# Optimization experiments

Measured on AMD Instinct MI355X. Metric: run time of the kernel, lower is better.

The kernel has to match this reference:

```python
import jax, jax.numpy as jnp
import numpy as np

B, T, DIM = 8, 1024, 2048
H, NKV, HD = 16, 4, 128
G = H // NKV          # query heads per kv head
BASE = 10000.0
EPS = 1e-6
SCALE = HD ** -0.5


def _rope_tables(seqlen):
    inv = 1.0 / (BASE ** (np.arange(0, HD, 2, dtype=np.float32) / HD))  # [HD/2]
    t = np.arange(seqlen, dtype=np.float32)
    f = np.outer(t, inv)  # [T, HD/2]
    return jnp.asarray(np.cos(f)), jnp.asarray(np.sin(f))


def _rms_norm(x):
    return x * jax.lax.rsqrt(jnp.mean(x * x, axis=-1, keepdims=True) + EPS)


def _rope(x, cos, sin):
    # x: [B, heads, T, HD]; cos/sin broadcast over batch and heads
    x1, x2 = x[..., : HD // 2], x[..., HD // 2 :]
    return jnp.concatenate([x1 * cos - x2 * sin, x2 * cos + x1 * sin], axis=-1)


def setup_inputs() -> dict:
    key = jax.random.key(0)
    ks = jax.random.split(key, 6)
    s = 1.0 / np.sqrt(DIM)
    return {
        "x": jax.random.normal(ks[0], (B, T, DIM), dtype=jnp.float32),
        "Wq": jax.random.normal(ks[1], (DIM, DIM), dtype=jnp.float32) * s,
        "Wk": jax.random.normal(ks[2], (NKV * HD, DIM), dtype=jnp.float32) * s,
        "Wv": jax.random.normal(ks[3], (NKV * HD, DIM), dtype=jnp.float32) * s,
        "Wproj": jax.random.normal(ks[4], (DIM, DIM), dtype=jnp.float32) * s,
        "q_gain": jnp.ones((H,), dtype=jnp.float32),
    }


def reference(x, Wq, Wk, Wv, Wproj, q_gain):
    bsz, seqlen, dim = x.shape
    # projections -> [B, heads, T, HD]
    q = (x @ Wq.T).reshape(bsz, seqlen, H, HD).transpose(0, 2, 1, 3)
    k = (x @ Wk.T).reshape(bsz, seqlen, NKV, HD).transpose(0, 2, 1, 3)
    v = (x @ Wv.T).reshape(bsz, seqlen, NKV, HD).transpose(0, 2, 1, 3)

    cos, sin = _rope_tables(seqlen)
    cos, sin = cos[None, None], sin[None, None]
    q = _rope(_rms_norm(q), cos, sin) * q_gain[None, :, None, None]
    k = _rope(_rms_norm(k), cos, sin)

    # GQA: group query heads instead of materializing repeated k/v
    qg = q.reshape(bsz, NKV, G, seqlen, HD)
    scores = jnp.einsum("bngtd,bnsd->bngts", qg, k) * SCALE  # [B,NKV,G,T,T]
    causal = jnp.tril(jnp.ones((seqlen, seqlen), dtype=bool))
    scores = jnp.where(causal, scores, jnp.finfo(scores.dtype).min)
    p = jax.nn.softmax(scores, axis=-1)
    y = jnp.einsum("bngts,bnsd->bngtd", p, v)  # [B,NKV,G,T,HD]
    y = y.transpose(0, 3, 1, 2, 4).reshape(bsz, seqlen, dim)

    # XSA: subtract self-value projection per kv head
    y_g = y.reshape(bsz, seqlen, NKV, G, HD)
    v_t = v.transpose(0, 2, 1, 3)  # [B,T,NKV,HD]
    vn = v_t / (jnp.linalg.norm(v_t, axis=-1, keepdims=True) + 1e-8)
    vn = vn[:, :, :, None, :]  # broadcast over group dim
    proj_comp = jnp.sum(y_g * vn, axis=-1, keepdims=True) * vn
    y = (y_g - proj_comp).reshape(bsz, seqlen, dim)

    return y @ Wproj.T
```

## Files before the change

### kernel.cpp

```cpp
#include <hip/hip_runtime.h>
#include <stdint.h>

#define T_SEQ 1024

typedef _Float16 f16x8 __attribute__((ext_vector_type(8)));
typedef _Float16 f16x2 __attribute__((ext_vector_type(2)));
typedef float f32x4 __attribute__((ext_vector_type(4)));

typedef __attribute__((address_space(1))) const uint8_t* gptr_t;
typedef __attribute__((address_space(3))) uint8_t* lptr_t;

__device__ __forceinline__ void gload16(const _Float16* g, _Float16* l) {
  __builtin_amdgcn_global_load_lds((gptr_t)g, (lptr_t)l, 16, 0, 0);
}

__global__ __launch_bounds__(256) void convert_all(
    const float* __restrict__ x, const float* __restrict__ Wq,
    const float* __restrict__ Wk, const float* __restrict__ Wv,
    const float* __restrict__ Wp, _Float16* __restrict__ xh,
    _Float16* __restrict__ wqh, _Float16* __restrict__ wkh,
    _Float16* __restrict__ wvh, _Float16* __restrict__ wph) {
  int i = blockIdx.x * 256 + threadIdx.x;
  const float* in;
  _Float16* out;
  int base;
  if (i < 2097152)      { in = x;  out = xh;  base = 0; }
  else if (i < 2621440) { in = Wq; out = wqh; base = 2097152; }
  else if (i < 2752512) { in = Wk; out = wkh; base = 2621440; }
  else if (i < 2883584) { in = Wv; out = wvh; base = 2752512; }
  else                  { in = Wp; out = wph; base = 2883584; }
  int j = i - base;
  const float4* p = (const float4*)in + (size_t)j * 2;
  float4 a = p[0], b = p[1];
  f16x8 o;
  o[0] = (_Float16)a.x; o[1] = (_Float16)a.y; o[2] = (_Float16)a.z; o[3] = (_Float16)a.w;
  o[4] = (_Float16)b.x; o[5] = (_Float16)b.y; o[6] = (_Float16)b.z; o[7] = (_Float16)b.w;
  ((f16x8*)out)[j] = o;
}

template <typename OutT>
__global__ __launch_bounds__(512, 2) void gemm256(
    const _Float16* __restrict__ A, const _Float16* __restrict__ B,
    OutT* __restrict__ C0, int ldc0, int nb0,
    OutT* __restrict__ C1, int ldc1, int nbn) {
  __shared__ _Float16 As[2][256][64];
  __shared__ _Float16 Bs[2][256][64];
  const int tid = threadIdx.x;
  const int wave = tid >> 6, lane = tid & 63;
  const int lm = lane & 15, lq = lane >> 4;
  const int wm = wave >> 2, wn = wave & 3;

  const int qx = (int)gridDim.x >> 3;
  const int swz = ((int)blockIdx.x & 7) * qx + ((int)blockIdx.x >> 3);
  const int bm = swz / nbn, bn = swz % nbn;

  const int r8 = lane >> 3;
  const int csw = ((lane & 7) ^ r8) * 8;
  const _Float16* Asrc = A + (size_t)(bm * 256 + wave * 16 + r8) * 2048 + csw;
  const _Float16* Bsrc = B + (size_t)(bn * 256 + wave * 16 + r8) * 2048 + csw;

  f32x4 acc[8][4];
#pragma unroll
  for (int m = 0; m < 8; m++)
#pragma unroll
    for (int n = 0; n < 4; n++) acc[m][n] = (f32x4){0.f, 0.f, 0.f, 0.f};

  f16x8 af[4][2], bf[4][2];

  auto stageA = [&](int t, int h) {
    const _Float16* s = Asrc + (size_t)h * 128 * 2048 + t * 64;
    _Float16* d = &As[t & 1][h * 128 + wave * 16][0];
    gload16(s, d);
    gload16(s + (size_t)8 * 2048, d + 8 * 64);
  };
  auto stageB = [&](int t, int h) {
    const _Float16* s = Bsrc + (size_t)h * 128 * 2048 + t * 64;
    _Float16* d = &Bs[t & 1][h * 128 + wave * 16][0];
    gload16(s, d);
    gload16(s + (size_t)8 * 2048, d + 8 * 64);
  };
  auto lda = [&](int b, int mh) {
#pragma unroll
    for (int m = 0; m < 4; m++)
#pragma unroll
      for (int ks = 0; ks < 2; ks++)
        af[m][ks] = *(const f16x8*)&As[b][wm * 128 + mh * 64 + m * 16 + lm]
                                      [(((ks * 4 + lq)) ^ (lm & 7)) * 8];
  };
  auto ldb = [&](int b, int nh) {
#pragma unroll
    for (int n = 0; n < 2; n++)
#pragma unroll
      for (int ks = 0; ks < 2; ks++)
        bf[nh * 2 + n][ks] = *(const f16x8*)&Bs[b][wn * 64 + nh * 32 + n * 16 + lm]
                                               [(((ks * 4 + lq)) ^ (lm & 7)) * 8];
  };
  auto mfmaQ = [&](int mh, int nh) {
    __builtin_amdgcn_s_setprio(1);
#pragma unroll
    for (int m = 0; m < 4; m++)
#pragma unroll
      for (int n = 0; n < 2; n++)
#pragma unroll
        for (int ks = 0; ks < 2; ks++)
          acc[mh * 4 + m][nh * 2 + n] = __builtin_amdgcn_mfma_f32_16x16x32_f16(
              af[m][ks], bf[nh * 2 + n][ks], acc[mh * 4 + m][nh * 2 + n], 0, 0, 0);
    __builtin_amdgcn_s_setprio(0);
  };

#define BAR() __builtin_amdgcn_s_barrier()
#define BARX()                                         \
  do {                                                 \
    asm volatile("s_waitcnt lgkmcnt(0)" ::: "memory"); \
    __builtin_amdgcn_s_barrier();                      \
  } while (0)

  stageA(0, 0); stageA(0, 1);
  stageB(0, 0); stageB(0, 1);
  stageB(1, 0); stageB(1, 1);
  asm volatile("s_waitcnt vmcnt(4)" ::: "memory");
  BAR();

  const int NT = 32;
  for (int j = 0; j < NT / 2; ++j) {
    const int t1 = 2 * j + 1, t2 = 2 * j + 2, t3 = 2 * j + 3;
    const bool s2 = t2 < NT, s3 = t3 < NT;
    lda(0, 0); ldb(0, 0); stageA(t1, 0);
    mfmaQ(0, 0);
    ldb(0, 1); stageA(t1, 1);
    mfmaQ(0, 1);
    lda(0, 1);
    mfmaQ(1, 0);
    BARX();
    if (s2) { stageB(t2, 0); stageB(t2, 1); }
    mfmaQ(1, 1);
    if (s2) { asm volatile("s_waitcnt vmcnt(4)" ::: "memory"); }
    else    { asm volatile("s_waitcnt vmcnt(0)" ::: "memory"); }
    BAR();
    lda(1, 0); ldb(1, 0); if (s2) stageA(t2, 0);
    mfmaQ(0, 0);
    ldb(1, 1); if (s2) stageA(t2, 1);
    mfmaQ(0, 1);
    lda(1, 1);
    mfmaQ(1, 0);
    BARX();
    if (s3) { stageB(t3, 0); stageB(t3, 1); }
    mfmaQ(1, 1);
    asm volatile("s_waitcnt vmcnt(4)" ::: "memory");
    BAR();
  }
#undef BAR
#undef BARX

  OutT* C;
  int ldc, cb;
  if (bn < nb0) { C = C0; ldc = ldc0; cb = bn * 256; }
  else          { C = C1; ldc = ldc1; cb = (bn - nb0) * 256; }
#pragma unroll
  for (int m = 0; m < 8; m++) {
    size_t gr = (size_t)(bm * 256 + wm * 128 + m * 16 + lq * 4);
#pragma unroll
    for (int n = 0; n < 4; n++) {
      int gc = cb + wn * 64 + n * 16 + lm;
#pragma unroll
      for (int r = 0; r < 4; r++)
        C[(gr + r) * ldc + gc] = (OutT)acc[m][n][r];
    }
  }
}

__global__ __launch_bounds__(256) void transpose16(const _Float16* __restrict__ in,
                                                   _Float16* __restrict__ out) {
  __shared__ _Float16 Ts[64][72];
  int tr = blockIdx.x * 64, tc = blockIdx.y * 64;
  int r0 = threadIdx.x >> 3, c8 = (threadIdx.x & 7) * 8;
#pragma unroll
  for (int i = 0; i < 2; i++) {
    int r = r0 + i * 32;
    *(f16x8*)&Ts[r][c8] = *(const f16x8*)&in[(size_t)(tr + r) * 1024 + tc + c8];
  }
  __syncthreads();
#pragma unroll
  for (int i = 0; i < 2; i++) {
    int oc = r0 + i * 32;
    f16x8 o;
#pragma unroll
    for (int j = 0; j < 8; j++) o[j] = Ts[c8 + j][oc];
    *(f16x8*)&out[(size_t)(tc + oc) * 8192 + tr + c8] = o;
  }
}

__global__ __launch_bounds__(256) void rmsrope_all(_Float16* __restrict__ qh,
                                                   _Float16* __restrict__ kvb,
                                                   const float* __restrict__ gain) {
  int gw = blockIdx.x * 4 + (threadIdx.x >> 6);
  int lane = threadIdx.x & 63;
  _Float16* row;
  int t;
  float g = 1.0f;
  if (gw < 131072) {
    int h = gw & 15;
    t = (gw >> 4) & 1023;
    row = qh + (size_t)gw * 128;
    g = gain[h] * 0.08838834764831845f * 1.4426950408889634f;
  } else {
    int gk = gw - 131072;
    t = (gk >> 2) & 1023;
    row = kvb + (size_t)(gk >> 2) * 1024 + (gk & 3) * 128;
  }
  float x1 = (float)row[lane], x2 = (float)row[lane + 64];
  float ss = x1 * x1 + x2 * x2;
#pragma unroll
  for (int m = 1; m < 64; m <<= 1) ss += __shfl_xor(ss, m);
  float scale = rsqrtf(ss * (1.0f / 128.0f) + 1e-6f) * g;
  float inv = exp2f((float)lane * -0.2076205059304601f);
  float ang = (float)t * inv;
  float c = cosf(ang), s = sinf(ang);
  row[lane]      = (_Float16)((x1 * c - x2 * s) * scale);
  row[lane + 64] = (_Float16)((x2 * c + x1 * s) * scale);
}

__global__ __launch_bounds__(256, 2) void attn_mfma(const _Float16* __restrict__ q,
                                                    const _Float16* __restrict__ k,
                                                    const _Float16* __restrict__ vT,
                                                    _Float16* __restrict__ y) {
  __shared__ _Float16 Ks[2][4][64][32];
  __shared__ _Float16 VTs[2][2][128][32];
  __shared__ _Float16 Ps[4][32][64];
  int h = blockIdx.y, b = blockIdx.z;
  int kvh = h >> 2;
  int tid = threadIdx.x, wave = tid >> 6, lane = tid & 63;
  int lm = lane & 15, lq = lane >> 4;
  int srow = lane >> 2, scol = (lane & 3) * 8;

  for (int pass = 0; pass < 2; ++pass) {
    int qt = pass ? (int)blockIdx.x : 7 - (int)blockIdx.x;

    f16x8 qf[2][4];
#pragma unroll
    for (int mt = 0; mt < 2; mt++) {
      const _Float16* qp =
          q + ((size_t)((b * T_SEQ + qt * 128 + wave * 32 + mt * 16 + lm) * 16 + h)) * 128 +
          lq * 8;
#pragma unroll
      for (int ks = 0; ks < 4; ks++) qf[mt][ks] = *(const f16x8*)(qp + ks * 32);
    }

    f32x4 O[2][8];
#pragma unroll
    for (int mt = 0; mt < 2; mt++)
#pragma unroll
      for (int i = 0; i < 8; i++) O[mt][i] = (f32x4){0.f, 0.f, 0.f, 0.f};
    float mrow[2][4], lrow[2][4];
#pragma unroll
    for (int mt = 0; mt < 2; mt++)
#pragma unroll
      for (int r = 0; r < 4; r++) { mrow[mt][r] = -1e30f; lrow[mt][r] = 0.f; }

    const _Float16* kg =
        k + (size_t)(b * T_SEQ + srow) * 1024 + kvh * 128 + wave * 32 + scol;
    const _Float16* vg =
        vT + (size_t)(kvh * 128 + (wave >> 1) * 64 + srow) * 8192 + b * T_SEQ +
        (wave & 1) * 32 + scol;

    int wrow = qt * 128 + wave * 32;
    int nit = (qt + 1) * 2;

#pragma unroll
    for (int i = 0; i < 4; i++) {
      gload16(kg + (size_t)i * 16 * 1024, &Ks[0][wave][i * 16][0]);
      gload16(vg + (size_t)i * 16 * 8192, &VTs[0][wave & 1][(wave >> 1) * 64 + i * 16][0]);
    }
    kg += (size_t)64 * 1024;
    vg += 64;
    asm volatile("s_waitcnt vmcnt(0)" ::: "memory");
    __builtin_amdgcn_s_barrier();

    for (int it = 0; it < nit; ++it) {
      int cur = it & 1;
      int s0 = it * 64;
      if (it + 1 < nit) {
#pragma unroll
        for (int i = 0; i < 4; i++) {
          gload16(kg + (size_t)i * 16 * 1024, &Ks[cur ^ 1][wave][i * 16][0]);
          gload16(vg + (size_t)i * 16 * 8192,
                  &VTs[cur ^ 1][wave & 1][(wave >> 1) * 64 + i * 16][0]);
        }
        kg += (size_t)64 * 1024;
        vg += 64;
      }

      f32x4 S[2][4];
#pragma unroll
      for (int mt = 0; mt < 2; mt++)
#pragma unroll
        for (int ct = 0; ct < 4; ct++) S[mt][ct] = (f32x4){0.f, 0.f, 0.f, 0.f};
      __builtin_amdgcn_s_setprio(1);
#pragma unroll
      for (int ct = 0; ct < 4; ct++)
#pragma unroll
        for (int ks = 0; ks < 4; ks++) {
          f16x8 bfr = *(const f16x8*)&Ks[cur][ks][ct * 16 + lm][lq * 8];
          S[0][ct] = __builtin_amdgcn_mfma_f32_16x16x32_f16(qf[0][ks], bfr, S[0][ct], 0, 0, 0);
          S[1][ct] = __builtin_amdgcn_mfma_f32_16x16x32_f16(qf[1][ks], bfr, S[1][ct], 0, 0, 0);
        }
      __builtin_amdgcn_s_setprio(0);

      float p[2][4][4], al[2][4];
#pragma unroll
      for (int mt = 0; mt < 2; mt++) {
        bool need_mask = (s0 + 63 > wrow + mt * 16);
#pragma unroll
        for (int r = 0; r < 4; r++) {
          int grow = wrow + mt * 16 + lq * 4 + r;
          float mx = -1e30f;
#pragma unroll
          for (int ct = 0; ct < 4; ct++) {
            float sv = S[mt][ct][r];
            if (need_mask && (s0 + ct * 16 + lm > grow)) sv = -1e30f;
            p[mt][r][ct] = sv;
            mx = fmaxf(mx, sv);
          }
#pragma unroll
          for (int m = 1; m < 16; m <<= 1) mx = fmaxf(mx, __shfl_xor(mx, m));
          float mn = fmaxf(mrow[mt][r], mx);
          float a = exp2f(mrow[mt][r] - mn);
          mrow[mt][r] = mn;
          float rs = 0.f;
#pragma unroll
          for (int ct = 0; ct < 4; ct++) {
            float pv = exp2f(p[mt][r][ct] - mn);
            p[mt][r][ct] = pv;
            rs += pv;
          }
#pragma unroll
          for (int m = 1; m < 16; m <<= 1) rs += __shfl_xor(rs, m);
          lrow[mt][r] = lrow[mt][r] * a + rs;
          al[mt][r] = a;
        }
      }

#pragma unroll
      for (int mt = 0; mt < 2; mt++)
#pragma unroll
        for (int r = 0; r < 4; r++) {
          int prow = mt * 16 + lq * 4 + r;
#pragma unroll
          for (int ct = 0; ct < 4; ct++) {
            int cg = (ct * 2 + (lm >> 3)) ^ (prow & 7);
            Ps[wave][prow][cg * 8 + (lm & 7)] = (_Float16)p[mt][r][ct];
          }
        }
#pragma unroll
      for (int mt = 0; mt < 2; mt++)
#pragma unroll
        for (int ct = 0; ct < 8; ct++)
#pragma unroll
          for (int r = 0; r < 4; r++) O[mt][ct][r] *= al[mt][r];

#pragma unroll
      for (int ks2 = 0; ks2 < 2; ks2++) {
        f16x8 afr[2];
#pragma unroll
        for (int mt = 0; mt < 2; mt++) {
          int prow = mt * 16 + lm;
          int cg = (ks2 * 4 + lq) ^ (prow & 7);
          afr[mt] = *(const f16x8*)&Ps[wave][prow][cg * 8];
        }
        __builtin_amdgcn_s_setprio(1);
#pragma unroll
        for (int ct = 0; ct < 8; ct++) {
          f16x8 bfr = *(const f16x8*)&VTs[cur][ks2][ct * 16 + lm][lq * 8];
          O[0][ct] = __builtin_amdgcn_mfma_f32_16x16x32_f16(afr[0], bfr, O[0][ct], 0, 0, 0);
          O[1][ct] = __builtin_amdgcn_mfma_f32_16x16x32_f16(afr[1], bfr, O[1][ct], 0, 0, 0);
        }
        __builtin_amdgcn_s_setprio(0);
      }
      asm volatile("s_waitcnt vmcnt(0)" ::: "memory");
      __builtin_amdgcn_s_barrier();
    }

#pragma unroll
    for (int mt = 0; mt < 2; mt++) {
      float linv[4];
#pragma unroll
      for (int r = 0; r < 4; r++) linv[r] = 1.0f / lrow[mt][r];
      int qrow_base = wrow + mt * 16 + lq * 4;
#pragma unroll
      for (int ct = 0; ct < 8; ct++)
#pragma unroll
        for (int r = 0; r < 4; r++)
          y[((size_t)(b * T_SEQ + qrow_base + r) * 16 + h) * 128 + ct * 16 + lm] =
              (_Float16)(O[mt][ct][r] * linv[r]);
    }
  }
}

__global__ __launch_bounds__(256) void vreject(const _Float16* __restrict__ y,
                                               const _Float16* __restrict__ kvb,
                                               _Float16* __restrict__ yh) {
  int gw = blockIdx.x * 4 + (threadIdx.x >> 6);
  int lane = threadIdx.x & 63;
  int bt = gw >> 2, n = gw & 3;
  const f16x2* vrow = (const f16x2*)(kvb + (size_t)bt * 1024 + 512 + n * 128);
  f16x2 vv = vrow[lane];
  float v0 = (float)vv[0], v1 = (float)vv[1];
  float ss = v0 * v0 + v1 * v1;
#pragma unroll
  for (int m = 1; m < 64; m <<= 1) ss += __shfl_xor(ss, m);
  float invn = 1.0f / (sqrtf(ss) + 1e-8f);
  float n0 = v0 * invn, n1 = v1 * invn;
  const _Float16* ybase = y + (size_t)bt * 2048 + n * 512;
  _Float16* obase = yh + (size_t)bt * 2048 + n * 512;
#pragma unroll
  for (int g = 0; g < 4; g++) {
    f16x2 yy = ((const f16x2*)(ybase + g * 128))[lane];
    float y0 = (float)yy[0], y1 = (float)yy[1];
    float d = y0 * n0 + y1 * n1;
#pragma unroll
    for (int m = 1; m < 64; m <<= 1) d += __shfl_xor(d, m);
    f16x2 oo;
    oo[0] = (_Float16)(y0 - d * n0);
    oo[1] = (_Float16)(y1 - d * n1);
    ((f16x2*)(obase + g * 128))[lane] = oo;
  }
}

extern "C" void kernel_launch(void* const* d_in, const int* in_sizes, int n_in,
                              void* d_out, int out_size, void* d_ws, size_t ws_size,
                              hipStream_t stream) {
  const float* x    = (const float*)d_in[0];
  const float* Wq   = (const float*)d_in[1];
  const float* Wk   = (const float*)d_in[2];
  const float* Wv   = (const float*)d_in[3];
  const float* Wp   = (const float*)d_in[4];
  const float* gain = (const float*)d_in[5];
  float* out = (float*)d_out;

  char* w = (char*)d_ws;
  _Float16* xh   = (_Float16*)(w + 0);
  _Float16* wqh  = (_Float16*)(w + 32u * 1048576);
  _Float16* wkvh = (_Float16*)(w + 40u * 1048576);
  _Float16* wph  = (_Float16*)(w + 44u * 1048576);
  _Float16* qh   = (_Float16*)(w + 52u * 1048576);
  _Float16* kvb  = (_Float16*)(w + 84u * 1048576);
  _Float16* vTg  = (_Float16*)(w + 100u * 1048576);
  _Float16* ya   = (_Float16*)(w + 108u * 1048576);
  _Float16* yh2  = xh;

  convert_all<<<13312, 256, 0, stream>>>(x, Wq, Wk, Wv, Wp, xh, wqh,
                                         wkvh, wkvh + (size_t)512 * 2048, wph);

  gemm256<_Float16><<<384, 512, 0, stream>>>(xh, wqh, qh, 2048, 8, kvb, 1024, 12);

  transpose16<<<dim3(128, 8), 256, 0, stream>>>(kvb + 512, vTg);
  rmsrope_all<<<40960, 256, 0, stream>>>(qh, kvb, gain);

  attn_mfma<<<dim3(4, 16, 8), 256, 0, stream>>>(qh, kvb, vTg, ya);

  vreject<<<8192, 256, 0, stream>>>(ya, kvb, yh2);

  gemm256<float><<<256, 512, 0, stream>>>(yh2, wph, out, 2048, 8,
                                          (float*)nullptr, 2048, 8);
}
```

Baseline: 459.0 us.

## Merge transpose and rmsrope kernels; read V fragments directly from global memory

Folds the V transpose into the RMS-norm/RoPE kernel as extra blocks so one launch replaces two. In attention, the double-buffered V tile in LDS is removed and each wave loads its V^T MFMA operands straight from global memory (relying on L2/L1 reuse across the four query heads sharing a kv head). This cuts LDS usage and async copies, which may raise occupancy. In exchange the global loads now sit in the MFMA critical path with latency that is not prefetched.

```diff
diff --git a/kernel.cpp b/kernel.cpp
--- a/kernel.cpp
+++ b/kernel.cpp
@@ -169,31 +169,33 @@
   }
 }
 
-__global__ __launch_bounds__(256) void transpose16(const _Float16* __restrict__ in,
-                                                   _Float16* __restrict__ out) {
+__global__ __launch_bounds__(256) void prep_all(const _Float16* __restrict__ vin,
+                                                _Float16* __restrict__ vTg,
+                                                _Float16* __restrict__ qh,
+                                                _Float16* __restrict__ kvb,
+                                                const float* __restrict__ gain) {
   __shared__ _Float16 Ts[64][72];
-  int tr = blockIdx.x * 64, tc = blockIdx.y * 64;
-  int r0 = threadIdx.x >> 3, c8 = (threadIdx.x & 7) * 8;
-#pragma unroll
-  for (int i = 0; i < 2; i++) {
-    int r = r0 + i * 32;
-    *(f16x8*)&Ts[r][c8] = *(const f16x8*)&in[(size_t)(tr + r) * 1024 + tc + c8];
-  }
-  __syncthreads();
-#pragma unroll
-  for (int i = 0; i < 2; i++) {
-    int oc = r0 + i * 32;
-    f16x8 o;
-#pragma unroll
-    for (int j = 0; j < 8; j++) o[j] = Ts[c8 + j][oc];
-    *(f16x8*)&out[(size_t)(tc + oc) * 8192 + tr + c8] = o;
-  }
-}
-
-__global__ __launch_bounds__(256) void rmsrope_all(_Float16* __restrict__ qh,
-                                                   _Float16* __restrict__ kvb,
-                                                   const float* __restrict__ gain) {
-  int gw = blockIdx.x * 4 + (threadIdx.x >> 6);
+  int bid = blockIdx.x;
+  if (bid < 1024) {
+    int tr = (bid & 127) * 64, tc = (bid >> 7) * 64;
+    int r0 = threadIdx.x >> 3, c8 = (threadIdx.x & 7) * 8;
+#pragma unroll
+    for (int i = 0; i < 2; i++) {
+      int r = r0 + i * 32;
+      *(f16x8*)&Ts[r][c8] = *(const f16x8*)&vin[(size_t)(tr + r) * 1024 + tc + c8];
+    }
+    __syncthreads();
+#pragma unroll
+    for (int i = 0; i < 2; i++) {
+      int oc = r0 + i * 32;
+      f16x8 o;
+#pragma unroll
+      for (int j = 0; j < 8; j++) o[j] = Ts[c8 + j][oc];
+      *(f16x8*)&vTg[(size_t)(tc + oc) * 8192 + tr + c8] = o;
+    }
+    return;
+  }
+  int gw = (bid - 1024) * 4 + (threadIdx.x >> 6);
   int lane = threadIdx.x & 63;
   _Float16* row;
   int t;
@@ -225,7 +227,6 @@
                                                     const _Float16* __restrict__ vT,
                                                     _Float16* __restrict__ y) {
   __shared__ _Float16 Ks[2][4][64][32];
-  __shared__ _Float16 VTs[2][2][128][32];
   __shared__ _Float16 Ps[4][32][64];
   int h = blockIdx.y, b = blockIdx.z;
   int kvh = h >> 2;
@@ -233,6 +234,9 @@
   int lm = lane & 15, lq = lane >> 4;
   int srow = lane >> 2, scol = (lane & 3) * 8;
 
+  const _Float16* vbase =
+      vT + (size_t)(kvh * 128 + lm) * 8192 + b * T_SEQ + lq * 8;
+
   for (int pass = 0; pass < 2; ++pass) {
     int qt = pass ? (int)blockIdx.x : 7 - (int)blockIdx.x;
 
@@ -259,20 +263,14 @@
 
     const _Float16* kg =
         k + (size_t)(b * T_SEQ + srow) * 1024 + kvh * 128 + wave * 32 + scol;
-    const _Float16* vg =
-        vT + (size_t)(kvh * 128 + (wave >> 1) * 64 + srow) * 8192 + b * T_SEQ +
-        (wave & 1) * 32 + scol;
 
     int wrow = qt * 128 + wave * 32;
     int nit = (qt + 1) * 2;
 
 #pragma unroll
-    for (int i = 0; i < 4; i++) {
+    for (int i = 0; i < 4; i++)
       gload16(kg + (size_t)i * 16 * 1024, &Ks[0][wave][i * 16][0]);
-      gload16(vg + (size_t)i * 16 * 8192, &VTs[0][wave & 1][(wave >> 1) * 64 + i * 16][0]);
-    }
     kg += (size_t)64 * 1024;
-    vg += 64;
     asm volatile("s_waitcnt vmcnt(0)" ::: "memory");
     __builtin_amdgcn_s_barrier();
 
@@ -281,13 +279,9 @@
       int s0 = it * 64;
       if (it + 1 < nit) {
 #pragma unroll
-        for (int i = 0; i < 4; i++) {
+        for (int i = 0; i < 4; i++)
           gload16(kg + (size_t)i * 16 * 1024, &Ks[cur ^ 1][wave][i * 16][0]);
-          gload16(vg + (size_t)i * 16 * 8192,
-                  &VTs[cur ^ 1][wave & 1][(wave >> 1) * 64 + i * 16][0]);
-        }
         kg += (size_t)64 * 1024;
-        vg += 64;
       }
 
       f32x4 S[2][4];
@@ -358,6 +352,7 @@
 #pragma unroll
           for (int r = 0; r < 4; r++) O[mt][ct][r] *= al[mt][r];
 
+      const _Float16* vs = vbase + s0;
 #pragma unroll
       for (int ks2 = 0; ks2 < 2; ks2++) {
         f16x8 afr[2];
@@ -370,7 +365,7 @@
         __builtin_amdgcn_s_setprio(1);
 #pragma unroll
         for (int ct = 0; ct < 8; ct++) {
-          f16x8 bfr = *(const f16x8*)&VTs[cur][ks2][ct * 16 + lm][lq * 8];
+          f16x8 bfr = *(const f16x8*)(vs + (size_t)(ct * 16) * 8192 + ks2 * 32);
           O[0][ct] = __builtin_amdgcn_mfma_f32_16x16x32_f16(afr[0], bfr, O[0][ct], 0, 0, 0);
           O[1][ct] = __builtin_amdgcn_mfma_f32_16x16x32_f16(afr[1], bfr, O[1][ct], 0, 0, 0);
         }
@@ -453,8 +448,7 @@
 
   gemm256<_Float16><<<384, 512, 0, stream>>>(xh, wqh, qh, 2048, 8, kvb, 1024, 12);
 
-  transpose16<<<dim3(128, 8), 256, 0, stream>>>(kvb + 512, vTg);
-  rmsrope_all<<<40960, 256, 0, stream>>>(qh, kvb, gain);
+  prep_all<<<41984, 256, 0, stream>>>(kvb + 512, vTg, qh, kvb, gain);
 
   attn_mfma<<<dim3(4, 16, 8), 256, 0, stream>>>(qh, kvb, vTg, ya);
 
```

Measured after the change: 499.9 us. 1.09x slower.
